# Performance work log

Measured on AMD Instinct MI355X. Metric: run time of the kernel, lower is better.

## Reference

```python
import jax, jax.numpy as jnp
import numpy as np

NUM_CLASSES = 19
RMI_RADIUS = 3
POOL_SIZE = 3
POOL_STRIDE = 3
IGNORE_INDEX = 255
LOSS_WEIGHT = 1.0


def _avg_pool_nchw(x, k, s):
    # torch F.avg_pool2d with padding=k//2, count_include_pad=True
    p = k // 2
    summed = jax.lax.reduce_window(
        x, 0.0, jax.lax.add,
        window_dimensions=(1, 1, k, k),
        window_strides=(1, 1, s, s),
        padding=[(0, 0), (0, 0), (p, p), (p, p)])
    return summed / float(k * k)


def _map_get_pairs(labels, probs, radius):
    h, w = labels.shape[2], labels.shape[3]
    nh, nw = h - radius + 1, w - radius + 1
    la = jnp.stack([labels[:, :, y:y + nh, x:x + nw]
                    for y in range(radius) for x in range(radius)], axis=2)
    pr = jnp.stack([probs[:, :, y:y + nh, x:x + nw]
                    for y in range(radius) for x in range(radius)], axis=2)
    return la, pr  # (N, C, r*r, nh, nw)


def _log_det_by_cholesky(mat):
    chol = jnp.linalg.cholesky(mat)
    diag = jnp.diagonal(chol, axis1=-2, axis2=-1)
    return 2.0 * jnp.sum(jnp.log(diag + 1e-8), axis=-1)


def _rmi_lower_bound(labels_4d, probs_4d):
    labels_4d = _avg_pool_nchw(labels_4d, POOL_SIZE, POOL_STRIDE)
    probs_4d = _avg_pool_nchw(probs_4d, POOL_SIZE, POOL_STRIDE)
    la, pr = _map_get_pairs(labels_4d, probs_4d, RMI_RADIUS)
    N, C, D = la.shape[:3]
    la = la.reshape(N, C, D, -1)   # (N, C, D, M)
    pr = pr.reshape(N, C, D, -1)
    M = la.shape[-1]
    la = la - la.mean(axis=-1, keepdims=True)
    pr = pr - pr.mean(axis=-1, keepdims=True)
    la_cov = jnp.einsum('ncdm,ncem->ncde', la, la) / M
    pr_cov = jnp.einsum('ncdm,ncem->ncde', pr, pr) / M
    pr_la_cov = jnp.einsum('ncdm,ncem->ncde', pr, la) / M
    eye = jnp.eye(D, dtype=la_cov.dtype)
    la_cov_inv = jnp.linalg.inv(la_cov + eye * 1e-5)
    appro_var = pr_cov - jnp.einsum('ncde,ncef,ncgf->ncdg',
                                    pr_la_cov, la_cov_inv, pr_la_cov)
    appro_var = appro_var + eye * 1e-6
    rmi_per_class = 0.5 * _log_det_by_cholesky(appro_var)  # (N, C)
    rmi_per_class = rmi_per_class.mean(axis=0)             # (C,)
    return jnp.sum(rmi_per_class) / NUM_CLASSES


def setup_inputs() -> dict:
    key = jax.random.key(0)
    k1, k2 = jax.random.split(key)
    cls_score = jax.random.normal(k1, (4, 19, 512, 512), dtype=jnp.float32)
    label = jax.random.randint(k2, (4, 512, 512), 0, NUM_CLASSES, dtype=jnp.int64)
    return {"cls_score": cls_score, "label": label}


def reference(cls_score, label):
    probs = jax.nn.softmax(cls_score.astype(jnp.float32), axis=1)
    valid = (label >= 0) & (label < NUM_CLASSES) & (label != IGNORE_INDEX)
    lbl = jnp.where(valid, label, 0)
    onehot = jax.nn.one_hot(lbl, NUM_CLASSES, dtype=jnp.float32)
    onehot = jnp.transpose(onehot, (0, 3, 1, 2))  # (N, C, H, W)
    vmask = valid[:, None, :, :].astype(jnp.float32)
    onehot = onehot * vmask
    probs = probs * vmask
    loss = _rmi_lower_bound(onehot, probs)
    return LOSS_WEIGHT * loss
```

## Files before the change

### kernel.cpp

```cpp
#include <hip/hip_runtime.h>
#include <math.h>

#define NBATCH 4
#define NCLS   19
#define HWDIM  512
#define HW     (512 * 512)
#define PH     171
#define PHP    176
#define PP2A   (171 * 176)
#define NHW    169
#define MM     (169 * 169)
#define NBAND  11
#define NSTRIP 43
#define ZS     2

typedef float f4 __attribute__((ext_vector_type(4)));
typedef float f2 __attribute__((ext_vector_type(2)));

__global__ __launch_bounds__(512) void stage1_pool(
    const float* __restrict__ cls, const int* __restrict__ label,
    float* __restrict__ P, float* __restrict__ L) {
  int n  = blockIdx.x / PH;
  int ph = blockIdx.x - n * PH;
  int col = threadIdx.x;

  float vv[3][NCLS];
  int lbs[3];
#pragma unroll
  for (int i = 0; i < 3; ++i) {
    int r = 3 * ph - 1 + i;
    bool ok = (r >= 0) && (r < HWDIM);
    if (ok) {
      lbs[i] = label[((size_t)n * HWDIM + r) * HWDIM + col];
      const float* base = cls + (size_t)n * NCLS * HW + (size_t)r * HWDIM + col;
#pragma unroll
      for (int c = 0; c < NCLS; ++c) vv[i][c] = base[(size_t)c * HW];
    } else {
      lbs[i] = -1;
#pragma unroll
      for (int c = 0; c < NCLS; ++c) vv[i][c] = 0.f;
    }
  }

  float accP[NCLS], accL[NCLS];
#pragma unroll
  for (int c = 0; c < NCLS; ++c) { accP[c] = 0.f; accL[c] = 0.f; }
#pragma unroll
  for (int i = 0; i < 3; ++i) {
    int lb = lbs[i];
    float mx = vv[i][0];
#pragma unroll
    for (int c = 1; c < NCLS; ++c) mx = fmaxf(mx, vv[i][c]);
    float se = 0.f;
    float ex[NCLS];
#pragma unroll
    for (int c = 0; c < NCLS; ++c) {
      ex[c] = __expf(vv[i][c] - mx);
      se += ex[c];
    }
    float m = (lb >= 0 && lb < NCLS) ? 1.f : 0.f;
    float inv = m / se;
#pragma unroll
    for (int c = 0; c < NCLS; ++c) {
      accP[c] += ex[c] * inv;
      accL[c] += (lb == c) ? 1.f : 0.f;
    }
  }

  __shared__ float xbP[10][516];
  __shared__ float xbL[10][516];
  const float inv9 = 1.f / 9.f;
#pragma unroll
  for (int c0 = 0; c0 < NCLS; c0 += 10) {
#pragma unroll
    for (int cc = 0; cc < 10; ++cc) {
      if (c0 + cc < NCLS) {
        xbP[cc][1 + col] = accP[(c0 + cc) < NCLS ? (c0 + cc) : 0];
        xbL[cc][1 + col] = accL[(c0 + cc) < NCLS ? (c0 + cc) : 0];
        if (col == 0) { xbP[cc][0] = 0.f; xbL[cc][0] = 0.f; }
      }
    }
    __syncthreads();
    if (col < PH) {
      int pw = col;
#pragma unroll
      for (int cc = 0; cc < 10; ++cc) {
        if (c0 + cc < NCLS) {
          int c = c0 + cc;
          float sP = xbP[cc][3 * pw] + xbP[cc][3 * pw + 1] + xbP[cc][3 * pw + 2];
          float sL = xbL[cc][3 * pw] + xbL[cc][3 * pw + 1] + xbL[cc][3 * pw + 2];
          size_t o = ((size_t)(n * NCLS + c)) * PP2A + (size_t)ph * PHP + pw;
          P[o] = sP * inv9;
          L[o] = sL * inv9;
        }
      }
    } else if (col < PHP) {
#pragma unroll
      for (int cc = 0; cc < 10; ++cc) {
        if (c0 + cc < NCLS) {
          int c = c0 + cc;
          size_t o = ((size_t)(n * NCLS + c)) * PP2A + (size_t)ph * PHP + col;
          P[o] = 0.f;
          L[o] = 0.f;
        }
      }
    }
    __syncthreads();
  }
}

template <int PART, int NA, int POS>
__device__ __forceinline__ void fma_pos(float (&acc)[NA],
                                        const float (&wp)[18],
                                        const float (&wl)[18]) {
  if (PART == 0) {
#pragma unroll
    for (int d = 0; d < 9; ++d) {
      acc[d]     += wl[(d / 3) * 6 + POS + (d % 3)];
      acc[9 + d] += wp[(d / 3) * 6 + POS + (d % 3)];
    }
    int k = 18;
#pragma unroll
    for (int d = 0; d < 9; ++d)
#pragma unroll
      for (int e = d; e < 9; ++e) {
        acc[k] += wl[(d / 3) * 6 + POS + (d % 3)] *
                  wl[(e / 3) * 6 + POS + (e % 3)];
        ++k;
      }
  } else if (PART == 1) {
    int k = 0;
#pragma unroll
    for (int d = 0; d < 9; ++d)
#pragma unroll
      for (int e = d; e < 9; ++e) {
        acc[k] += wp[(d / 3) * 6 + POS + (d % 3)] *
                  wp[(e / 3) * 6 + POS + (e % 3)];
        ++k;
      }
  } else {
#pragma unroll
    for (int d = 0; d < 9; ++d)
#pragma unroll
      for (int e = 0; e < 9; ++e)
        acc[d * 9 + e] += wp[(d / 3) * 6 + POS + (d % 3)] *
                          wl[(e / 3) * 6 + POS + (e % 3)];
  }
}

template <int PART>
__device__ __forceinline__ void mom_body(
    const float* __restrict__ Pp, const float* __restrict__ Lp,
    float* __restrict__ covp, int rec, int z, float* red) {
  constexpr int NA  = (PART == 0) ? 63 : (PART == 1 ? 45 : 81);
  constexpr int OFF = (PART == 0) ? 0  : (PART == 1 ? 63 : 108);

  float acc[NA];
#pragma unroll
  for (int k = 0; k < NA; ++k) acc[k] = 0.f;

  int tid = threadIdx.x;
  if (tid < NSTRIP * NBAND) {
    int b  = tid / NSTRIP;
    int s  = tid - b * NSTRIP;
    int x0 = 4 * s;
    int zr0 = (NHW * z) / ZS;
    int zr1 = (NHW * (z + 1)) / ZS;
    int zr  = zr1 - zr0;
    int y0 = zr0 + (zr * b) / NBAND;
    int y1 = zr0 + (zr * (b + 1)) / NBAND;

    float wp[18], wl[18];
#pragma unroll
    for (int r = 0; r < 3; ++r) {
      const float* rp = Pp + (y0 + r) * PHP + x0;
      *(f4*)&wp[r * 6]     = *(const f4*)rp;
      *(f2*)&wp[r * 6 + 4] = *(const f2*)(rp + 4);
      if (PART != 1) {
        const float* rl = Lp + (y0 + r) * PHP + x0;
        *(f4*)&wl[r * 6]     = *(const f4*)rl;
        *(f2*)&wl[r * 6 + 4] = *(const f2*)(rl + 4);
      }
    }

    if (x0 + 4 <= NHW) {
      for (int y = y0; y < y1; ++y) {
        int yn = (y + 3 <= PH - 1) ? (y + 3) : (PH - 1);
        const float* rp = Pp + yn * PHP + x0;
        f4 tp4 = *(const f4*)rp;
        f2 tp2 = *(const f2*)(rp + 4);
        f4 tl4; f2 tl2;
        if (PART != 1) {
          const float* rl = Lp + yn * PHP + x0;
          tl4 = *(const f4*)rl;
          tl2 = *(const f2*)(rl + 4);
        }
        fma_pos<PART, NA, 0>(acc, wp, wl);
        fma_pos<PART, NA, 1>(acc, wp, wl);
        fma_pos<PART, NA, 2>(acc, wp, wl);
        fma_pos<PART, NA, 3>(acc, wp, wl);
#pragma unroll
        for (int t = 0; t < 12; ++t) {
          wp[t] = wp[t + 6];
          if (PART != 1) wl[t] = wl[t + 6];
        }
        *(f4*)&wp[12] = tp4;
        *(f2*)&wp[16] = tp2;
        if (PART != 1) { *(f4*)&wl[12] = tl4; *(f2*)&wl[16] = tl2; }
      }
    } else {
      for (int y = y0; y < y1; ++y) {
        int yn = (y + 3 <= PH - 1) ? (y + 3) : (PH - 1);
        const float* rp = Pp + yn * PHP + x0;
        f4 tp4 = *(const f4*)rp;
        f2 tp2 = *(const f2*)(rp + 4);
        f4 tl4; f2 tl2;
        if (PART != 1) {
          const float* rl = Lp + yn * PHP + x0;
          tl4 = *(const f4*)rl;
          tl2 = *(const f2*)(rl + 4);
        }
        fma_pos<PART, NA, 0>(acc, wp, wl);
#pragma unroll
        for (int t = 0; t < 12; ++t) {
          wp[t] = wp[t + 6];
          if (PART != 1) wl[t] = wl[t + 6];
        }
        *(f4*)&wp[12] = tp4;
        *(f2*)&wp[16] = tp2;
        if (PART != 1) { *(f4*)&wl[12] = tl4; *(f2*)&wl[16] = tl2; }
      }
    }
  }

  int lane = threadIdx.x & 63;
  int wid  = threadIdx.x >> 6;
#pragma unroll
  for (int k = 0; k < NA; ++k) {
    float v = acc[k];
    v += __shfl_down(v, 32, 64);
    v += __shfl_down(v, 16, 64);
    v += __shfl_down(v, 8, 64);
    if (lane < 8) red[(wid * 8 + lane) * 84 + k] = v;
  }
  __syncthreads();
  if (tid < NA) {
    float sm = 0.f;
#pragma unroll
    for (int w = 0; w < 64; ++w) sm += red[w * 84 + tid];
    covp[(size_t)rec * 192 + OFF + tid] = sm;
  }
}

__global__ __launch_bounds__(512) void stage2_mom(
    const float* __restrict__ P, const float* __restrict__ L,
    float* __restrict__ covp) {
  __shared__ float red[64 * 84];
  int nc = blockIdx.x;
  int z  = blockIdx.z;
  int rec = z * (NBATCH * NCLS) + nc;
  const float* Pp = P + (size_t)nc * PP2A;
  const float* Lp = L + (size_t)nc * PP2A;
  if (blockIdx.y == 0)      mom_body<0>(Pp, Lp, covp, rec, z, red);
  else if (blockIdx.y == 1) mom_body<1>(Pp, Lp, covp, rec, z, red);
  else                      mom_body<2>(Pp, Lp, covp, rec, z, red);
}

__global__ __launch_bounds__(64) void stage3_rmi(float* __restrict__ covp) {
  int nc  = blockIdx.x;
  int tid = threadIdx.x;
  const float* s0 = covp + (size_t)nc * 192;
  const float* s1 = covp + ((size_t)NBATCH * NCLS + nc) * 192;
  __shared__ double lc[81], pc[81], plc[81], mla[9], mpr[9];
  const double Minv = 1.0 / (double)MM;
#define LDM(k) ((double)s0[k] + (double)s1[k])

  if (tid < 9)       mla[tid]     = LDM(tid) * Minv;
  else if (tid < 18) mpr[tid - 9] = LDM(tid) * Minv;
  __syncthreads();

  for (int e = tid; e < 81; e += 64) {
    int r = e / 9, c = e - 9 * (e / 9);
    int lo = r < c ? r : c, hi = r < c ? c : r;
    int k = lo * 9 - lo * (lo - 1) / 2 + (hi - lo);
    double a = LDM(18 + k) * Minv - mla[r] * mla[c];
    if (r == c) a += 1e-5;
    lc[e] = a;
    pc[e] = LDM(63 + k) * Minv - mpr[r] * mpr[c];
    plc[e] = LDM(108 + e) * Minv - mpr[r] * mla[c];
  }
  __syncthreads();

  for (int j = 0; j < 9; ++j) {
    if (tid == 0) lc[j * 9 + j] = sqrt(lc[j * 9 + j]);
    __syncthreads();
    if (tid > j && tid < 9) lc[tid * 9 + j] /= lc[j * 9 + j];
    __syncthreads();
    if (tid > j && tid < 9) {
      double lij = lc[tid * 9 + j];
      for (int k = j + 1; k <= tid; ++k) lc[tid * 9 + k] -= lij * lc[k * 9 + j];
    }
    __syncthreads();
  }

  if (tid < 9) {
    int d = tid;
    for (int j = 0; j < 9; ++j) {
      double t = plc[d * 9 + j];
      for (int k = 0; k < j; ++k) t -= plc[d * 9 + k] * lc[j * 9 + k];
      plc[d * 9 + j] = t / lc[j * 9 + j];
    }
  }
  __syncthreads();

  for (int e = tid; e < 81; e += 64) {
    int r = e / 9, c = e - 9 * (e / 9);
    double a = pc[e];
    for (int f = 0; f < 9; ++f) a -= plc[r * 9 + f] * plc[c * 9 + f];
    if (r == c) a += 1e-6;
    pc[e] = a;
  }
  __syncthreads();

  for (int j = 0; j < 9; ++j) {
    if (tid == 0) pc[j * 9 + j] = sqrt(pc[j * 9 + j]);
    __syncthreads();
    if (tid > j && tid < 9) pc[tid * 9 + j] /= pc[j * 9 + j];
    __syncthreads();
    if (tid > j && tid < 9) {
      double lij = pc[tid * 9 + j];
      for (int k = j + 1; k <= tid; ++k) pc[tid * 9 + k] -= lij * pc[k * 9 + j];
    }
    __syncthreads();
  }

  if (tid == 0) {
    double sl = 0.0;
    for (int j = 0; j < 9; ++j) sl += log(pc[j * 9 + j] + 1e-8);
    *(double*)(covp + (size_t)nc * 192 + 190) = sl;
  }
#undef LDM
}

__global__ __launch_bounds__(64) void stage4_reduce(
    const float* __restrict__ covp, float* __restrict__ out) {
  int tid = threadIdx.x;
  double v = 0.0;
  if (tid < NBATCH * NCLS)
    v = *(const double*)(covp + (size_t)tid * 192 + 190);
  if (tid + 64 < NBATCH * NCLS)
    v += *(const double*)(covp + (size_t)(tid + 64) * 192 + 190);
#pragma unroll
  for (int o = 32; o > 0; o >>= 1) v += __shfl_down(v, o, 64);
  if (tid == 0) out[0] = (float)(v / (double)(NBATCH * NCLS));
}

extern "C" void kernel_launch(void* const* d_in, const int* in_sizes, int n_in,
                              void* d_out, int out_size, void* d_ws, size_t ws_size,
                              hipStream_t stream) {
  const float* cls  = (const float*)d_in[0];
  const int* label  = (const int*)d_in[1];
  float* out = (float*)d_out;

  float* P    = (float*)d_ws;
  float* L    = P + (size_t)NBATCH * NCLS * PP2A;
  float* covp = L + (size_t)NBATCH * NCLS * PP2A;

  stage1_pool<<<NBATCH * PH, 512, 0, stream>>>(cls, label, P, L);
  dim3 g2(NBATCH * NCLS, 3, ZS);
  stage2_mom<<<g2, 512, 0, stream>>>(P, L, covp);
  stage3_rmi<<<NBATCH * NCLS, 64, 0, stream>>>(covp);
  stage4_reduce<<<1, 64, 0, stream>>>(covp, out);
}
```

Before: 85.61 us.

## Compute shift-lag totals over full grid and correct borders in a separate kernel

Replaces the per-offset moment accumulation with lag-based autocorrelation totals computed over the whole pooled map. The 81/45/45 covariance entries collapse to 25 cross lags and 13 self lags. A new assembly kernel subtracts the edge rows and columns each window offset excludes, using boundary strips cached in shared memory. This removes the redundant FMAs across the 9 window shifts and the z-split of the grid, at the cost of an extra launch, a serial border-correction pass and a small guard zone in the workspace.

```diff
diff --git a/kernel.cpp b/kernel.cpp
--- a/kernel.cpp
+++ b/kernel.cpp
@@ -10,16 +10,16 @@
 #define PP2A   (171 * 176)
 #define NHW    169
 #define MM     (169 * 169)
-#define NBAND  11
-#define NSTRIP 43
-#define ZS     2
-
-typedef float f4 __attribute__((ext_vector_type(4)));
-typedef float f2 __attribute__((ext_vector_type(2)));
+#define NNC    (NBATCH * NCLS)
+
+typedef float f4  __attribute__((ext_vector_type(4)));
+typedef float f2v __attribute__((ext_vector_type(2)));
 
 __global__ __launch_bounds__(512) void stage1_pool(
     const float* __restrict__ cls, const int* __restrict__ label,
-    float* __restrict__ P, float* __restrict__ L) {
+    float* __restrict__ guard, float* __restrict__ P, float* __restrict__ L) {
+  if (blockIdx.x == 0 && threadIdx.x < 16) guard[threadIdx.x] = 0.f;
+
   int n  = blockIdx.x / PH;
   int ph = blockIdx.x - n * PH;
   int col = threadIdx.x;
@@ -109,185 +109,402 @@
   }
 }
 
-template <int PART, int NA, int POS>
-__device__ __forceinline__ void fma_pos(float (&acc)[NA],
-                                        const float (&wp)[18],
-                                        const float (&wl)[18]) {
-  if (PART == 0) {
-#pragma unroll
-    for (int d = 0; d < 9; ++d) {
-      acc[d]     += wl[(d / 3) * 6 + POS + (d % 3)];
-      acc[9 + d] += wp[(d / 3) * 6 + POS + (d % 3)];
-    }
-    int k = 18;
-#pragma unroll
-    for (int d = 0; d < 9; ++d)
-#pragma unroll
-      for (int e = d; e < 9; ++e) {
-        acc[k] += wl[(d / 3) * 6 + POS + (d % 3)] *
-                  wl[(e / 3) * 6 + POS + (e % 3)];
-        ++k;
-      }
-  } else if (PART == 1) {
-    int k = 0;
-#pragma unroll
-    for (int d = 0; d < 9; ++d)
-#pragma unroll
-      for (int e = d; e < 9; ++e) {
-        acc[k] += wp[(d / 3) * 6 + POS + (d % 3)] *
-                  wp[(e / 3) * 6 + POS + (e % 3)];
-        ++k;
-      }
+__device__ __forceinline__ void ldrow7(f2v (&W)[7], const float* X, int row,
+                                       int x0) {
+  if (row >= 0 && row <= 170) {
+    const float* p = X + (ptrdiff_t)row * PHP + x0;
+    f2v a = *(const f2v*)(p - 2);
+    f2v b = *(const f2v*)(p);
+    f2v c = *(const f2v*)(p + 2);
+    f2v d = *(const f2v*)(p + 4);
+    W[0] = a; W[2] = b; W[4] = c; W[6] = d;
+    W[1] = (f2v){a.y, b.x}; W[3] = (f2v){b.y, c.x}; W[5] = (f2v){c.y, d.x};
   } else {
 #pragma unroll
-    for (int d = 0; d < 9; ++d)
-#pragma unroll
-      for (int e = 0; e < 9; ++e)
-        acc[d * 9 + e] += wp[(d / 3) * 6 + POS + (d % 3)] *
-                          wl[(e / 3) * 6 + POS + (e % 3)];
-  }
-}
-
-template <int PART>
-__device__ __forceinline__ void mom_body(
-    const float* __restrict__ Pp, const float* __restrict__ Lp,
-    float* __restrict__ covp, int rec, int z, float* red) {
-  constexpr int NA  = (PART == 0) ? 63 : (PART == 1 ? 45 : 81);
-  constexpr int OFF = (PART == 0) ? 0  : (PART == 1 ? 63 : 108);
-
-  float acc[NA];
-#pragma unroll
-  for (int k = 0; k < NA; ++k) acc[k] = 0.f;
-
-  int tid = threadIdx.x;
-  if (tid < NSTRIP * NBAND) {
-    int b  = tid / NSTRIP;
-    int s  = tid - b * NSTRIP;
-    int x0 = 4 * s;
-    int zr0 = (NHW * z) / ZS;
-    int zr1 = (NHW * (z + 1)) / ZS;
-    int zr  = zr1 - zr0;
-    int y0 = zr0 + (zr * b) / NBAND;
-    int y1 = zr0 + (zr * (b + 1)) / NBAND;
-
-    float wp[18], wl[18];
-#pragma unroll
-    for (int r = 0; r < 3; ++r) {
-      const float* rp = Pp + (y0 + r) * PHP + x0;
-      *(f4*)&wp[r * 6]     = *(const f4*)rp;
-      *(f2*)&wp[r * 6 + 4] = *(const f2*)(rp + 4);
-      if (PART != 1) {
-        const float* rl = Lp + (y0 + r) * PHP + x0;
-        *(f4*)&wl[r * 6]     = *(const f4*)rl;
-        *(f2*)&wl[r * 6 + 4] = *(const f2*)(rl + 4);
-      }
-    }
-
-    if (x0 + 4 <= NHW) {
-      for (int y = y0; y < y1; ++y) {
-        int yn = (y + 3 <= PH - 1) ? (y + 3) : (PH - 1);
-        const float* rp = Pp + yn * PHP + x0;
-        f4 tp4 = *(const f4*)rp;
-        f2 tp2 = *(const f2*)(rp + 4);
-        f4 tl4; f2 tl2;
-        if (PART != 1) {
-          const float* rl = Lp + yn * PHP + x0;
-          tl4 = *(const f4*)rl;
-          tl2 = *(const f2*)(rl + 4);
-        }
-        fma_pos<PART, NA, 0>(acc, wp, wl);
-        fma_pos<PART, NA, 1>(acc, wp, wl);
-        fma_pos<PART, NA, 2>(acc, wp, wl);
-        fma_pos<PART, NA, 3>(acc, wp, wl);
-#pragma unroll
-        for (int t = 0; t < 12; ++t) {
-          wp[t] = wp[t + 6];
-          if (PART != 1) wl[t] = wl[t + 6];
-        }
-        *(f4*)&wp[12] = tp4;
-        *(f2*)&wp[16] = tp2;
-        if (PART != 1) { *(f4*)&wl[12] = tl4; *(f2*)&wl[16] = tl2; }
-      }
-    } else {
-      for (int y = y0; y < y1; ++y) {
-        int yn = (y + 3 <= PH - 1) ? (y + 3) : (PH - 1);
-        const float* rp = Pp + yn * PHP + x0;
-        f4 tp4 = *(const f4*)rp;
-        f2 tp2 = *(const f2*)(rp + 4);
-        f4 tl4; f2 tl2;
-        if (PART != 1) {
-          const float* rl = Lp + yn * PHP + x0;
-          tl4 = *(const f4*)rl;
-          tl2 = *(const f2*)(rl + 4);
-        }
-        fma_pos<PART, NA, 0>(acc, wp, wl);
-#pragma unroll
-        for (int t = 0; t < 12; ++t) {
-          wp[t] = wp[t + 6];
-          if (PART != 1) wl[t] = wl[t + 6];
-        }
-        *(f4*)&wp[12] = tp4;
-        *(f2*)&wp[16] = tp2;
-        if (PART != 1) { *(f4*)&wl[12] = tl4; *(f2*)&wl[16] = tl2; }
-      }
-    }
-  }
-
-  int lane = threadIdx.x & 63;
-  int wid  = threadIdx.x >> 6;
+    for (int j = 0; j < 7; ++j) W[j] = (f2v){0.f, 0.f};
+  }
+}
+
+__device__ __forceinline__ void ldy2(f2v& a, f2v& b, const float* Y, int row,
+                                     int x0) {
+  const float* p = Y + (size_t)row * PHP + x0;
+  a = *(const f2v*)p;
+  b = *(const f2v*)(p + 2);
+}
+
+__device__ __forceinline__ void fma_self13(f2v (&acc)[14],
+    const f2v (&c0)[7], const f2v (&c1)[7], const f2v (&c2)[7]) {
+  acc[13] += c0[2]; acc[13] += c0[4];
+#pragma unroll
+  for (int i = 0; i < 3; ++i) {
+    acc[i] += c0[2] * c0[2 + i];
+    acc[i] += c0[4] * c0[4 + i];
+  }
+#pragma unroll
+  for (int k = 0; k < 5; ++k) {
+    acc[3 + k] += c0[2] * c1[k];
+    acc[3 + k] += c0[4] * c1[k + 2];
+  }
+#pragma unroll
+  for (int k = 0; k < 5; ++k) {
+    acc[8 + k] += c0[2] * c2[k];
+    acc[8 + k] += c0[4] * c2[k + 2];
+  }
+}
+
+__device__ __forceinline__ void fma_cross25(f2v (&acc)[25],
+    const f2v& ya, const f2v& yb,
+    const f2v (&m2)[7], const f2v (&m1)[7], const f2v (&z0)[7],
+    const f2v (&p1)[7], const f2v (&p2)[7]) {
+#pragma unroll
+  for (int k = 0; k < 5; ++k) {
+    acc[k]      += ya * m2[k]; acc[k]      += yb * m2[k + 2];
+    acc[5 + k]  += ya * m1[k]; acc[5 + k]  += yb * m1[k + 2];
+    acc[10 + k] += ya * z0[k]; acc[10 + k] += yb * z0[k + 2];
+    acc[15 + k] += ya * p1[k]; acc[15 + k] += yb * p1[k + 2];
+    acc[20 + k] += ya * p2[k]; acc[20 + k] += yb * p2[k + 2];
+  }
+}
+
+template <int NA>
+__device__ __forceinline__ void epi_tot(f2v (&acc)[NA], float* red,
+                                        float* __restrict__ tot, int nc,
+                                        int mode ) {
+  int tid  = threadIdx.x;
+  int lane = tid & 63;
+  int wid  = tid >> 6;
 #pragma unroll
   for (int k = 0; k < NA; ++k) {
-    float v = acc[k];
+    float v = acc[k].x + acc[k].y;
     v += __shfl_down(v, 32, 64);
     v += __shfl_down(v, 16, 64);
     v += __shfl_down(v, 8, 64);
-    if (lane < 8) red[(wid * 8 + lane) * 84 + k] = v;
+    if (lane < 8) red[(wid * 8 + lane) * 28 + k] = v;
   }
   __syncthreads();
   if (tid < NA) {
     float sm = 0.f;
 #pragma unroll
-    for (int w = 0; w < 64; ++w) sm += red[w * 84 + tid];
-    covp[(size_t)rec * 192 + OFF + tid] = sm;
-  }
-}
-
-__global__ __launch_bounds__(512) void stage2_mom(
+    for (int w = 0; w < 64; ++w) sm += red[w * 28 + tid];
+    int off;
+    if (mode == 2)      off = 28 + tid;
+    else if (tid < 13)  off = (mode ? 15 : 2) + tid;
+    else                off = mode ? 1 : 0;
+    tot[(size_t)nc * 64 + off] = sm;
+  }
+}
+
+__device__ void self_tot(const float* __restrict__ X, float* __restrict__ tot,
+                         int nc, float* red, int mode) {
+  f2v acc[14];
+#pragma unroll
+  for (int k = 0; k < 14; ++k) acc[k] = (f2v){0.f, 0.f};
+  int tid = threadIdx.x;
+  if (tid < 473) {
+    int b = tid / 43, s = tid - b * 43;
+    int x0 = 4 * s;
+    int u0 = (171 * b) / 11, u1 = (171 * (b + 1)) / 11;
+    f2v A[7], B[7], C[7], D[7];
+    ldrow7(A, X, u0, x0); ldrow7(B, X, u0 + 1, x0); ldrow7(C, X, u0 + 2, x0);
+    int span = u1 - u0, nf = span & ~3, u = u0;
+    for (int i = 0; i < nf; i += 4, u += 4) {
+      ldrow7(D, X, u + 3, x0); fma_self13(acc, A, B, C);
+      ldrow7(A, X, u + 4, x0); fma_self13(acc, B, C, D);
+      ldrow7(B, X, u + 5, x0); fma_self13(acc, C, D, A);
+      ldrow7(C, X, u + 6, x0); fma_self13(acc, D, A, B);
+    }
+    int r = span - nf;
+    if (r > 0) { ldrow7(D, X, u + 3, x0); fma_self13(acc, A, B, C); }
+    if (r > 1) { ldrow7(A, X, u + 4, x0); fma_self13(acc, B, C, D); }
+    if (r > 2) { fma_self13(acc, C, D, A); }
+  }
+  epi_tot<14>(acc, red, tot, nc, mode);
+}
+
+__device__ void cross_tot(const float* __restrict__ Y,
+                          const float* __restrict__ X,
+                          float* __restrict__ tot, int nc, float* red) {
+  f2v acc[25];
+#pragma unroll
+  for (int k = 0; k < 25; ++k) acc[k] = (f2v){0.f, 0.f};
+  int tid = threadIdx.x;
+  if (tid < 473) {
+    int b = tid / 43, s = tid - b * 43;
+    int x0 = 4 * s;
+    int u0 = (171 * b) / 11, u1 = (171 * (b + 1)) / 11;
+    f2v S0[7], S1[7], S2[7], S3[7], S4[7], S5[7];
+    f2v y0a, y0b, y1a, y1b;
+    ldrow7(S0, X, u0 - 2, x0); ldrow7(S1, X, u0 - 1, x0);
+    ldrow7(S2, X, u0, x0);     ldrow7(S3, X, u0 + 1, x0);
+    ldrow7(S4, X, u0 + 2, x0);
+    ldy2(y0a, y0b, Y, u0, x0);
+    int span = u1 - u0, nf = (span / 6) * 6, u = u0;
+    for (int i = 0; i < nf; i += 6, u += 6) {
+      ldrow7(S5, X, u + 3, x0); ldy2(y1a, y1b, Y, u + 1, x0);
+      fma_cross25(acc, y0a, y0b, S0, S1, S2, S3, S4);
+      ldrow7(S0, X, u + 4, x0); ldy2(y0a, y0b, Y, u + 2, x0);
+      fma_cross25(acc, y1a, y1b, S1, S2, S3, S4, S5);
+      ldrow7(S1, X, u + 5, x0); ldy2(y1a, y1b, Y, u + 3, x0);
+      fma_cross25(acc, y0a, y0b, S2, S3, S4, S5, S0);
+      ldrow7(S2, X, u + 6, x0); ldy2(y0a, y0b, Y, u + 4, x0);
+      fma_cross25(acc, y1a, y1b, S3, S4, S5, S0, S1);
+      ldrow7(S3, X, u + 7, x0); ldy2(y1a, y1b, Y, u + 5, x0);
+      fma_cross25(acc, y0a, y0b, S4, S5, S0, S1, S2);
+      ldrow7(S4, X, u + 8, x0); ldy2(y0a, y0b, Y, u + 6, x0);
+      fma_cross25(acc, y1a, y1b, S5, S0, S1, S2, S3);
+    }
+    int r = span - nf;
+    if (r > 0) { ldrow7(S5, X, u + 3, x0); ldy2(y1a, y1b, Y, u + 1, x0);
+                 fma_cross25(acc, y0a, y0b, S0, S1, S2, S3, S4); }
+    if (r > 1) { ldrow7(S0, X, u + 4, x0); ldy2(y0a, y0b, Y, u + 2, x0);
+                 fma_cross25(acc, y1a, y1b, S1, S2, S3, S4, S5); }
+    if (r > 2) { ldrow7(S1, X, u + 5, x0); ldy2(y1a, y1b, Y, u + 3, x0);
+                 fma_cross25(acc, y0a, y0b, S2, S3, S4, S5, S0); }
+    if (r > 3) { ldrow7(S2, X, u + 6, x0); ldy2(y0a, y0b, Y, u + 4, x0);
+                 fma_cross25(acc, y1a, y1b, S3, S4, S5, S0, S1); }
+    if (r > 4) { fma_cross25(acc, y0a, y0b, S4, S5, S0, S1, S2); }
+  }
+  epi_tot<25>(acc, red, tot, nc, 2);
+}
+
+__global__ __launch_bounds__(512) void stage2_tot(
     const float* __restrict__ P, const float* __restrict__ L,
-    float* __restrict__ covp) {
-  __shared__ float red[64 * 84];
+    float* __restrict__ tot) {
+  __shared__ float red[64 * 28];
   int nc = blockIdx.x;
-  int z  = blockIdx.z;
-  int rec = z * (NBATCH * NCLS) + nc;
-  const float* Pp = P + (size_t)nc * PP2A;
-  const float* Lp = L + (size_t)nc * PP2A;
-  if (blockIdx.y == 0)      mom_body<0>(Pp, Lp, covp, rec, z, red);
-  else if (blockIdx.y == 1) mom_body<1>(Pp, Lp, covp, rec, z, red);
-  else                      mom_body<2>(Pp, Lp, covp, rec, z, red);
+  const float* Xla = L + (size_t)nc * PP2A;
+  const float* Ypr = P + (size_t)nc * PP2A;
+  if (blockIdx.y == 0)      self_tot(Xla, tot, nc, red, 0);
+  else if (blockIdx.y == 1) self_tot(Ypr, tot, nc, red, 1);
+  else                      cross_tot(Ypr, Xla, tot, nc, red);
+}
+
+__global__ __launch_bounds__(512) void stage2b_asm(
+    const float* __restrict__ P, const float* __restrict__ L,
+    const float* __restrict__ tot, float* __restrict__ cov) {
+  __shared__ float rX[8 * 176], rY[8 * 176];
+  __shared__ float cX[12 * 171], cY[12 * 171];
+  __shared__ float sres[424];
+  int nc = blockIdx.x, tid = threadIdx.x;
+  const float* Xp = L + (size_t)nc * PP2A;
+  const float* Yp = P + (size_t)nc * PP2A;
+
+  for (int i = tid; i < 8 * 176; i += 512) {
+    int rr = i / 176, c = i - rr * 176;
+    int row = (rr < 4) ? rr : rr + 163;
+    rX[i] = Xp[(size_t)row * PHP + c];
+    rY[i] = Yp[(size_t)row * PHP + c];
+  }
+  for (int i = tid; i < 12 * 171; i += 512) {
+    int j = i / 171, u = i - j * 171;
+    int c = (j < 6) ? (j - 2) : (j + 161);
+    cX[i] = Xp[(ptrdiff_t)u * PHP + c];
+    cY[i] = Yp[(ptrdiff_t)u * PHP + c];
+  }
+  __syncthreads();
+
+  auto xri  = [](int r) { return (r < 4) ? r : r - 163; };
+  auto cidx = [](int c) { return (c <= 3) ? c + 2 : c - 161; };
+  auto Xv = [&](int r, int c) -> float {
+    if (r < 0 || r > 170 || c < 0) return 0.f;
+    return rX[xri(r) * 176 + c];
+  };
+  auto Yv = [&](int r, int c) -> float {
+    if (r < 0 || r > 170 || c < 0) return 0.f;
+    return rY[xri(r) * 176 + c];
+  };
+
+  if (tid < 424) {
+    float sum = 0.f;
+    if (tid < 200) {
+      int line = tid / 25, j = tid - line * 25;
+      int ay = j / 5 - 2, ax = (j % 5) - 2;
+      if (line < 4) {
+        int u = (line < 2) ? line : line + 167;
+        int ri = xri(u), r2 = u + ay;
+        if (r2 >= 0 && r2 <= 170) {
+          int ri2 = xri(r2);
+          for (int v = 0; v < 171; ++v) {
+            int c2 = v + ax;
+            float x = (c2 >= 0) ? rX[ri2 * 176 + c2] : 0.f;
+            sum += rY[ri * 176 + v] * x;
+          }
+        }
+      } else {
+        int v = ((line - 4) < 2) ? (line - 4) : (line - 4) + 167;
+        int yc = cidx(v), xc = cidx(v + ax);
+        for (int u = 0; u < 171; ++u) {
+          int r2 = u + ay;
+          float x = (r2 >= 0 && r2 <= 170) ? cX[xc * 171 + r2] : 0.f;
+          sum += cY[yc * 171 + u] * x;
+        }
+      }
+    } else if (tid < 304) {
+      int t2 = tid - 200;
+      int line = t2 / 13, j13 = t2 - line * 13;
+      int ay = (j13 < 3) ? 0 : ((j13 < 8) ? 1 : 2);
+      int ax = (j13 < 3) ? j13 : ((j13 < 8) ? j13 - 5 : j13 - 10);
+      if (line < 4) {
+        int u = (line < 2) ? line : line + 167;
+        int ri = xri(u), r2 = u + ay;
+        if (r2 <= 170) {
+          int ri2 = xri(r2);
+          for (int v = 0; v < 171; ++v) {
+            int c2 = v + ax;
+            float x = (c2 >= 0) ? rX[ri2 * 176 + c2] : 0.f;
+            sum += rX[ri * 176 + v] * x;
+          }
+        }
+      } else {
+        int v = ((line - 4) < 2) ? (line - 4) : (line - 4) + 167;
+        int c1 = cidx(v), c2i = cidx(v + ax);
+        for (int u = 0; u < 171; ++u) {
+          int r2 = u + ay;
+          float x = (r2 <= 170) ? cX[c2i * 171 + r2] : 0.f;
+          sum += cX[c1 * 171 + u] * x;
+        }
+      }
+    } else if (tid < 408) {
+      int t2 = tid - 304;
+      int line = t2 / 13, j13 = t2 - line * 13;
+      int ay = (j13 < 3) ? 0 : ((j13 < 8) ? 1 : 2);
+      int ax = (j13 < 3) ? j13 : ((j13 < 8) ? j13 - 5 : j13 - 10);
+      if (line < 4) {
+        int u = (line < 2) ? line : line + 167;
+        int ri = xri(u), r2 = u + ay;
+        if (r2 <= 170) {
+          int ri2 = xri(r2);
+          for (int v = 0; v < 171; ++v) {
+            int c2 = v + ax;
+            float y = (c2 >= 0) ? rY[ri2 * 176 + c2] : 0.f;
+            sum += rY[ri * 176 + v] * y;
+          }
+        }
+      } else {
+        int v = ((line - 4) < 2) ? (line - 4) : (line - 4) + 167;
+        int c1 = cidx(v), c2i = cidx(v + ax);
+        for (int u = 0; u < 171; ++u) {
+          int r2 = u + ay;
+          float y = (r2 <= 170) ? cY[c2i * 171 + r2] : 0.f;
+          sum += cY[c1 * 171 + u] * y;
+        }
+      }
+    } else if (tid < 416) {
+      int line = tid - 408;
+      if (line < 4) {
+        int u = (line < 2) ? line : line + 167;
+        int ri = xri(u);
+        for (int v = 0; v < 171; ++v) sum += rX[ri * 176 + v];
+      } else {
+        int v = ((line - 4) < 2) ? (line - 4) : (line - 4) + 167;
+        int xc = cidx(v);
+        for (int u = 0; u < 171; ++u) sum += cX[xc * 171 + u];
+      }
+    } else {
+      int line = tid - 416;
+      if (line < 4) {
+        int u = (line < 2) ? line : line + 167;
+        int ri = xri(u);
+        for (int v = 0; v < 171; ++v) sum += rY[ri * 176 + v];
+      } else {
+        int v = ((line - 4) < 2) ? (line - 4) : (line - 4) + 167;
+        int yc = cidx(v);
+        for (int u = 0; u < 171; ++u) sum += cY[yc * 171 + u];
+      }
+    }
+    sres[tid] = sum;
+  }
+  __syncthreads();
+
+  float* s = cov + (size_t)nc * 192;
+  const float* tt = tot + (size_t)nc * 64;
+  auto uline = [](int u) { return (u < 2) ? u : u - 167; };
+  const int ex0[3] = {169, 0, 0};
+  const int ex1[3] = {170, 170, 1};
+
+  if (tid < 81) {
+    int d = tid / 9, e = tid - 9 * d;
+    int dy = d / 3, dx = d - 3 * dy, ey = e / 3, ex = e - 3 * ey;
+    int ay = ey - dy, ax = ex - dx;
+    int j = (ay + 2) * 5 + (ax + 2);
+    int ra = ex0[dy], rb = ex1[dy], ca = ex0[dx], cb = ex1[dx];
+    float S = tt[28 + j];
+    S -= sres[uline(ra) * 25 + j] + sres[uline(rb) * 25 + j];
+    S -= sres[(4 + uline(ca)) * 25 + j] + sres[(4 + uline(cb)) * 25 + j];
+    S += Yv(ra, ca) * Xv(ra + ay, ca + ax) + Yv(ra, cb) * Xv(ra + ay, cb + ax);
+    S += Yv(rb, ca) * Xv(rb + ay, ca + ax) + Yv(rb, cb) * Xv(rb + ay, cb + ax);
+    s[108 + tid] = S;
+  } else if (tid < 126) {
+    int k = tid - 81, kk = k, d = 0;
+    while (kk >= 9 - d) { kk -= 9 - d; ++d; }
+    int e = d + kk;
+    int dy = d / 3, dx = d - 3 * dy, ey = e / 3, ex = e - 3 * ey;
+    int ay = ey - dy, ax = ex - dx;
+    int j13 = (ay == 0) ? ax : ((ay == 1) ? 5 + ax : 10 + ax);
+    int ra = ex0[dy], rb = ex1[dy], ca = ex0[dx], cb = ex1[dx];
+    float S = tt[2 + j13];
+    S -= sres[200 + uline(ra) * 13 + j13] + sres[200 + uline(rb) * 13 + j13];
+    S -= sres[200 + (4 + uline(ca)) * 13 + j13] +
+         sres[200 + (4 + uline(cb)) * 13 + j13];
+    S += Xv(ra, ca) * Xv(ra + ay, ca + ax) + Xv(ra, cb) * Xv(ra + ay, cb + ax);
+    S += Xv(rb, ca) * Xv(rb + ay, ca + ax) + Xv(rb, cb) * Xv(rb + ay, cb + ax);
+    s[18 + k] = S;
+  } else if (tid < 171) {
+    int k = tid - 126, kk = k, d = 0;
+    while (kk >= 9 - d) { kk -= 9 - d; ++d; }
+    int e = d + kk;
+    int dy = d / 3, dx = d - 3 * dy, ey = e / 3, ex = e - 3 * ey;
+    int ay = ey - dy, ax = ex - dx;
+    int j13 = (ay == 0) ? ax : ((ay == 1) ? 5 + ax : 10 + ax);
+    int ra = ex0[dy], rb = ex1[dy], ca = ex0[dx], cb = ex1[dx];
+    float S = tt[15 + j13];
+    S -= sres[304 + uline(ra) * 13 + j13] + sres[304 + uline(rb) * 13 + j13];
+    S -= sres[304 + (4 + uline(ca)) * 13 + j13] +
+         sres[304 + (4 + uline(cb)) * 13 + j13];
+    S += Yv(ra, ca) * Yv(ra + ay, ca + ax) + Yv(ra, cb) * Yv(ra + ay, cb + ax);
+    S += Yv(rb, ca) * Yv(rb + ay, ca + ax) + Yv(rb, cb) * Yv(rb + ay, cb + ax);
+    s[63 + k] = S;
+  } else if (tid < 180) {
+    int d = tid - 171;
+    int dy = d / 3, dx = d - 3 * dy;
+    int ra = ex0[dy], rb = ex1[dy], ca = ex0[dx], cb = ex1[dx];
+    float S = tt[0];
+    S -= sres[408 + uline(ra)] + sres[408 + uline(rb)];
+    S -= sres[408 + 4 + uline(ca)] + sres[408 + 4 + uline(cb)];
+    S += Xv(ra, ca) + Xv(ra, cb) + Xv(rb, ca) + Xv(rb, cb);
+    s[d] = S;
+  } else if (tid < 189) {
+    int d = tid - 180;
+    int dy = d / 3, dx = d - 3 * dy;
+    int ra = ex0[dy], rb = ex1[dy], ca = ex0[dx], cb = ex1[dx];
+    float S = tt[1];
+    S -= sres[416 + uline(ra)] + sres[416 + uline(rb)];
+    S -= sres[416 + 4 + uline(ca)] + sres[416 + 4 + uline(cb)];
+    S += Yv(ra, ca) + Yv(ra, cb) + Yv(rb, ca) + Yv(rb, cb);
+    s[9 + d] = S;
+  }
 }
 
 __global__ __launch_bounds__(64) void stage3_rmi(float* __restrict__ covp) {
   int nc  = blockIdx.x;
   int tid = threadIdx.x;
-  const float* s0 = covp + (size_t)nc * 192;
-  const float* s1 = covp + ((size_t)NBATCH * NCLS + nc) * 192;
+  const float* s = covp + (size_t)nc * 192;
   __shared__ double lc[81], pc[81], plc[81], mla[9], mpr[9];
   const double Minv = 1.0 / (double)MM;
-#define LDM(k) ((double)s0[k] + (double)s1[k])
-
-  if (tid < 9)       mla[tid]     = LDM(tid) * Minv;
-  else if (tid < 18) mpr[tid - 9] = LDM(tid) * Minv;
+
+  if (tid < 9)       mla[tid]     = (double)s[tid] * Minv;
+  else if (tid < 18) mpr[tid - 9] = (double)s[tid] * Minv;
   __syncthreads();
 
   for (int e = tid; e < 81; e += 64) {
     int r = e / 9, c = e - 9 * (e / 9);
     int lo = r < c ? r : c, hi = r < c ? c : r;
     int k = lo * 9 - lo * (lo - 1) / 2 + (hi - lo);
-    double a = LDM(18 + k) * Minv - mla[r] * mla[c];
+    double a = (double)s[18 + k] * Minv - mla[r] * mla[c];
     if (r == c) a += 1e-5;
     lc[e] = a;
-    pc[e] = LDM(63 + k) * Minv - mpr[r] * mpr[c];
-    plc[e] = LDM(108 + e) * Minv - mpr[r] * mla[c];
+    pc[e] = (double)s[63 + k] * Minv - mpr[r] * mpr[c];
+    plc[e] = (double)s[108 + e] * Minv - mpr[r] * mla[c];
   }
   __syncthreads();
 
@@ -339,20 +556,19 @@
     for (int j = 0; j < 9; ++j) sl += log(pc[j * 9 + j] + 1e-8);
     *(double*)(covp + (size_t)nc * 192 + 190) = sl;
   }
-#undef LDM
 }
 
 __global__ __launch_bounds__(64) void stage4_reduce(
     const float* __restrict__ covp, float* __restrict__ out) {
   int tid = threadIdx.x;
   double v = 0.0;
-  if (tid < NBATCH * NCLS)
+  if (tid < NNC)
     v = *(const double*)(covp + (size_t)tid * 192 + 190);
-  if (tid + 64 < NBATCH * NCLS)
+  if (tid + 64 < NNC)
     v += *(const double*)(covp + (size_t)(tid + 64) * 192 + 190);
 #pragma unroll
   for (int o = 32; o > 0; o >>= 1) v += __shfl_down(v, o, 64);
-  if (tid == 0) out[0] = (float)(v / (double)(NBATCH * NCLS));
+  if (tid == 0) out[0] = (float)(v / (double)NNC);
 }
 
 extern "C" void kernel_launch(void* const* d_in, const int* in_sizes, int n_in,
@@ -362,13 +578,16 @@
   const int* label  = (const int*)d_in[1];
   float* out = (float*)d_out;
 
-  float* P    = (float*)d_ws;
-  float* L    = P + (size_t)NBATCH * NCLS * PP2A;
-  float* covp = L + (size_t)NBATCH * NCLS * PP2A;
-
-  stage1_pool<<<NBATCH * PH, 512, 0, stream>>>(cls, label, P, L);
-  dim3 g2(NBATCH * NCLS, 3, ZS);
-  stage2_mom<<<g2, 512, 0, stream>>>(P, L, covp);
-  stage3_rmi<<<NBATCH * NCLS, 64, 0, stream>>>(covp);
-  stage4_reduce<<<1, 64, 0, stream>>>(covp, out);
-}
+  float* base = (float*)d_ws;
+  float* P    = base + 16;
+  float* L    = P + (size_t)NNC * PP2A;
+  float* tot  = L + (size_t)NNC * PP2A;
+  float* cov  = tot + (size_t)NNC * 64;
+
+  stage1_pool<<<NBATCH * PH, 512, 0, stream>>>(cls, label, base, P, L);
+  dim3 g2(NNC, 3, 1);
+  stage2_tot<<<g2, 512, 0, stream>>>(P, L, tot);
+  stage2b_asm<<<NNC, 512, 0, stream>>>(P, L, tot, cov);
+  stage3_rmi<<<NNC, 64, 0, stream>>>(cov);
+  stage4_reduce<<<1, 64, 0, stream>>>(cov, out);
+}
```

Result: faster. 83.31 us (-2.7%).
